# Optimization experiments

Hardware: AMD Instinct MI355X
Metric: run time of the kernel (lower is better)

The kernel has to match this reference:

```python
import jax, jax.numpy as jnp
import numpy as np

MAX_AREA_WIDTH = 3  # from init_kwargs


def _window_vals(val, width, merge):
    """Multi-scale forward window sums: for each w in 1..width, sum val[t:t+w]
    over the seq axis, concatenated along the seq axis (total length
    width*L - width*(width-1)/2). Equivalent to the torch recurrence."""
    B, H, L, D = val.shape
    csum = jnp.concatenate(
        [jnp.zeros((B, H, 1, D), val.dtype), jnp.cumsum(val, axis=2)], axis=2)
    parts = []
    for i in range(width):
        w = i + 1
        s = csum[:, :, w:, :] - csum[:, :, :L - w + 1, :]  # [B,H,L-i,D]
        if merge == 'mean':
            s = s / jnp.asarray(w, val.dtype)
        parts.append(s)
    return jnp.concatenate(parts, axis=2)


def _window_masks(mask, width, zero_pad):
    parts = [mask[:, :, :, i:] for i in range(width)]
    m = jnp.concatenate(parts, axis=-1)  # [B,H,L,L']
    if zero_pad:
        m = m.at[:, :, 0, :].set(0)
    return m


def setup_inputs() -> dict:
    key = jax.random.key(0)
    kq, kk, kv = jax.random.split(key, 3)
    B, H, L, D = 8, 8, 512, 64
    q = jax.random.normal(kq, (B, H, L, D), jnp.float32)
    k = jax.random.normal(kk, (B, H, L, D), jnp.float32)
    v = jax.random.normal(kv, (B, H, L, D), jnp.float32)
    # causal attention mask, as used in pykt knowledge-tracing models
    mask = jnp.broadcast_to(jnp.tril(jnp.ones((L, L), jnp.int32)), (B, H, L, L))
    return {"q": q, "k": k, "v": v, "d_k": 64, "mask": mask, "zero_pad": 1}


def reference(q, k, v, d_k, mask, zero_pad):
    W = MAX_AREA_WIDTH
    k_area = _window_vals(k, W, 'mean')   # [B,H,L',D]
    v_area = _window_vals(v, W, 'sum')    # [B,H,L',D]
    m = _window_masks(mask, W, zero_pad)  # [B,H,L,L']
    scores = jnp.einsum('bhqd,bhkd->bhqk', q, k_area) / jnp.sqrt(
        jnp.asarray(d_k, jnp.float32))
    scores = jnp.where(m == 0, jnp.asarray(-1e32, scores.dtype), scores)
    attn = jax.nn.softmax(scores, axis=-1)  # dropout omitted (eval / p=0)
    return jnp.einsum('bhqk,bhkd->bhqd', attn, v_area)
```

## Files before the change

kernel.cpp:

```cpp
#include <hip/hip_runtime.h>


#define LSEQ 512
#define DDIM 64
#define BQ 64
#define BK 64
#define NTH 256

__global__ __launch_bounds__(256, 2)
void area_attn_kernel(const float* __restrict__ qg,
                      const float* __restrict__ kg,
                      const float* __restrict__ vg,
                      float* __restrict__ outg) {
  const int bid = blockIdx.x;
  const int tid = threadIdx.x;

  __shared__ __align__(16) float Qs[64][68];
  __shared__ __align__(16) float KC[66 * 68];
  __shared__ __align__(16) float Ss[64][68];
  __shared__ __align__(16) float Vs[66][64];
  __shared__ float scale_arr[64];
  __shared__ float l_arr[64];

  if (bid >= 512) {
    const int bh = bid - 512;
    const float4* vb4 = (const float4*)(vg + (size_t)bh * LSEQ * DDIM);
    float4* red = (float4*)&Qs[0][0];
    const int d4 = tid & 15, rg = tid >> 4;
    float4 acc = make_float4(0.f, 0.f, 0.f, 0.f);
    for (int t = rg; t < LSEQ; t += 16) {
      float c = (t == 0 || t == LSEQ - 1) ? 3.f
              : (t == 1 || t == LSEQ - 2) ? 5.f : 6.f;
      float4 x = vb4[t * 16 + d4];
      acc.x += c * x.x; acc.y += c * x.y; acc.z += c * x.z; acc.w += c * x.w;
    }
    red[rg * 16 + d4] = acc;
    __syncthreads();
    if (rg == 0) {
      float4 s = make_float4(0.f, 0.f, 0.f, 0.f);
#pragma unroll
      for (int g = 0; g < 16; ++g) {
        float4 x = red[g * 16 + d4];
        s.x += x.x; s.y += x.y; s.z += x.z; s.w += x.w;
      }
      const float inv = 1.0f / 1533.0f;
      s.x *= inv; s.y *= inv; s.z *= inv; s.w *= inv;
      ((float4*)(outg + (size_t)bh * LSEQ * DDIM))[d4] = s;
    }
    return;
  }

  const int half = bid >> 8;
  const int qt = half ? (7 - (bid & 7)) : (bid & 7);
  const int bh = ((bid >> 3) & 31) + (half << 5);
  const int q0 = qt * BQ;

  const float* qb = qg + (size_t)bh * LSEQ * DDIM;
  const float* kb = kg + (size_t)bh * LSEQ * DDIM;
  const float* vb = vg + (size_t)bh * LSEQ * DDIM;

  {
    const float4* qa = (const float4*)(qb + q0 * DDIM);
#pragma unroll
    for (int it = 0; it < 4; ++it) {
      int f = tid + it * NTH;
      int r = f >> 4;
      int c4 = f & 15;
      float4 x = qa[f];
      int d0 = c4 * 4;
      Qs[d0 + 0][r] = x.x * 0.125f;
      Qs[d0 + 1][r] = x.y * 0.125f;
      Qs[d0 + 2][r] = x.z * 0.125f;
      Qs[d0 + 3][r] = x.w * 0.125f;
    }
  }

  const int ty = tid >> 4, tx = tid & 15;
  const int r0 = ty * 4, c0 = tx * 4;
  const int pr = tid >> 2, ps = tid & 3;
  const int ec0 = ps * 16;

  float Oa[4][4];
#pragma unroll
  for (int i = 0; i < 4; ++i)
#pragma unroll
    for (int j = 0; j < 4; ++j) Oa[i][j] = 0.f;
  float m_run = -3.0e38f, l_run = 0.f;

  const int ntiles = qt + 1;
  for (int kt = 0; kt < ntiles; ++kt) {
    const int t0 = kt * BK;

    if (ps == 0) {
      if (kt == 0) { Ss[pr][64] = -1.0e30f; Ss[pr][65] = -1.0e30f; }
      else         { Ss[pr][64] = Ss[pr][62]; Ss[pr][65] = Ss[pr][63]; }
    }
    __syncthreads();

    {
      const float4* ka = (const float4*)(kb + t0 * DDIM);
#pragma unroll
      for (int it = 0; it < 4; ++it) {
        int f = tid + it * NTH;
        int r = f >> 4;
        int c4 = f & 15;
        float4 x = ka[f];
        int d0 = c4 * 4;
        KC[(d0 + 0) * 68 + r] = x.x;
        KC[(d0 + 1) * 68 + r] = x.y;
        KC[(d0 + 2) * 68 + r] = x.z;
        KC[(d0 + 3) * 68 + r] = x.w;
      }
      const float4* va = (const float4*)(vb + t0 * DDIM);
#pragma unroll
      for (int it = 0; it < 4; ++it) {
        int f = tid + it * NTH;
        int r = f >> 4;
        int c4 = f & 15;
        ((float4*)Vs[r])[c4] = va[f];
      }
      if (tid < 32) {
        int rr = tid >> 4;
        int c4 = tid & 15;
        float4 x = make_float4(0.f, 0.f, 0.f, 0.f);
        if (kt > 0) x = ((const float4*)(vb + (size_t)(t0 - 2 + rr) * DDIM))[c4];
        ((float4*)Vs[64 + rr])[c4] = x;
      }
    }
    __syncthreads();

    {
      float acc[4][4];
#pragma unroll
      for (int i = 0; i < 4; ++i)
#pragma unroll
        for (int j = 0; j < 4; ++j) acc[i][j] = 0.f;
#pragma unroll 8
      for (int d = 0; d < 64; ++d) {
        float4 qv = *(const float4*)&Qs[d][r0];
        float4 kv = *(const float4*)&KC[d * 68 + c0];
        float qr[4] = {qv.x, qv.y, qv.z, qv.w};
        float kr[4] = {kv.x, kv.y, kv.z, kv.w};
#pragma unroll
        for (int i = 0; i < 4; ++i)
#pragma unroll
          for (int j = 0; j < 4; ++j) acc[i][j] = fmaf(qr[i], kr[j], acc[i][j]);
      }
#pragma unroll
      for (int i = 0; i < 4; ++i) {
        float4 o = make_float4(acc[i][0], acc[i][1], acc[i][2], acc[i][3]);
        *(float4*)&Ss[r0 + i][c0] = o;
      }
    }
    __syncthreads();

    {
      const int vmax = q0 + pr - t0;
      float pm1, pm2;
      if (ps == 0) { pm1 = Ss[pr][65]; pm2 = Ss[pr][64]; }
      else         { pm1 = Ss[pr][ec0 - 1]; pm2 = Ss[pr][ec0 - 2]; }

      float sv[16];
      *(float4*)&sv[0]  = *(const float4*)&Ss[pr][ec0];
      *(float4*)&sv[4]  = *(const float4*)&Ss[pr][ec0 + 4];
      *(float4*)&sv[8]  = *(const float4*)&Ss[pr][ec0 + 8];
      *(float4*)&sv[12] = *(const float4*)&Ss[pr][ec0 + 12];

      float mloc = -3.0e38f;
      {
        float a1 = pm1, a2 = pm2;
#pragma unroll
        for (int k = 0; k < 16; ++k) {
          float s0 = sv[k];
          float sc2 = 0.5f * (a1 + s0);
          float sc3 = (1.0f / 3.0f) * (a2 + a1 + s0);
          float mm = fmaxf(s0, fmaxf(sc2, sc3));
          if (ec0 + k <= vmax) mloc = fmaxf(mloc, mm);
          a2 = a1; a1 = s0;
        }
      }
      mloc = fmaxf(mloc, __shfl_xor(mloc, 1));
      mloc = fmaxf(mloc, __shfl_xor(mloc, 2));
      const float m_new = fmaxf(m_run, mloc);
      const float alpha = __expf(m_run - m_new);
      m_run = m_new;
      if (ps == 0) scale_arr[pr] = alpha;
      l_run *= alpha;

      float cf[18];
#pragma unroll
      for (int k = 0; k < 18; ++k) cf[k] = 0.f;
      float ladd = 0.f;
      {
        float a1 = pm1, a2 = pm2;
#pragma unroll
        for (int k = 0; k < 16; ++k) {
          float s0 = sv[k];
          bool vld = (ec0 + k) <= vmax;
          float p1 = vld ? __expf(s0 - m_new) : 0.f;
          float p2 = vld ? __expf(0.5f * (a1 + s0) - m_new) : 0.f;
          float p3 = vld ? __expf((1.0f / 3.0f) * (a2 + a1 + s0) - m_new) : 0.f;
          ladd += p1 + p2 + p3;
          cf[k + 2] += p1 + p2 + p3;
          cf[k + 1] += p2 + p3;
          cf[k]     += p3;
          a2 = a1; a1 = s0;
        }
      }
      ladd += __shfl_xor(ladd, 1);
      ladd += __shfl_xor(ladd, 2);
      l_run += ladd;
      if (ps == 0) l_arr[pr] = l_run;

      float up16 = __shfl_up(cf[16], 1, 4);
      float up17 = __shfl_up(cf[17], 1, 4);
      if (ps > 0) { cf[0] += up16; cf[1] += up17; }

#pragma unroll
      for (int k = 0; k < 16; ++k) {
        int lt = ec0 + k;
        int cc = (lt >= 2) ? (lt - 2) : (64 + lt);
        KC[cc * 68 + pr] = cf[k];
      }
      if (ps == 3) {
        KC[62 * 68 + pr] = cf[16];
        KC[63 * 68 + pr] = cf[17];
      }
    }
    __syncthreads();

    {
      float al[4];
#pragma unroll
      for (int i = 0; i < 4; ++i) al[i] = scale_arr[r0 + i];
#pragma unroll
      for (int i = 0; i < 4; ++i)
#pragma unroll
        for (int j = 0; j < 4; ++j) Oa[i][j] *= al[i];
#pragma unroll 2
      for (int cc = 0; cc < 66; ++cc) {
        float4 cv = *(const float4*)&KC[cc * 68 + r0];
        float4 vv = *(const float4*)&Vs[cc][c0];
        float cr[4] = {cv.x, cv.y, cv.z, cv.w};
        float vr[4] = {vv.x, vv.y, vv.z, vv.w};
#pragma unroll
        for (int i = 0; i < 4; ++i)
#pragma unroll
          for (int j = 0; j < 4; ++j) Oa[i][j] = fmaf(cr[i], vr[j], Oa[i][j]);
      }
    }
  }

  {
#pragma unroll
    for (int i = 0; i < 4; ++i) {
      int gr = q0 + r0 + i;
      if (gr != 0) {
        float inv = 1.0f / l_arr[r0 + i];
        float4 o = make_float4(Oa[i][0] * inv, Oa[i][1] * inv,
                               Oa[i][2] * inv, Oa[i][3] * inv);
        *(float4*)(outg + (size_t)(bh * LSEQ + gr) * DDIM + c0) = o;
      }
    }
  }
}

extern "C" void kernel_launch(void* const* d_in, const int* in_sizes, int n_in,
                              void* d_out, int out_size, void* d_ws, size_t ws_size,
                              hipStream_t stream) {
  (void)in_sizes; (void)n_in; (void)d_ws; (void)ws_size; (void)out_size;
  const float* q = (const float*)d_in[0];
  const float* k = (const float*)d_in[1];
  const float* v = (const float*)d_in[2];
  float* out = (float*)d_out;

  dim3 grid(512 + 64);
  area_attn_kernel<<<grid, NTH, 0, stream>>>(q, k, v, out);
}
```

Before: 177.0 us.

## Use bf16 MFMA for QK and PV with pre-transposed bf16 V

Replaces the fp32 scalar-FMA tile matmuls for QK^T and P·V with bf16 MFMA 16x16x32 instructions. A separate pre-kernel converts V to transposed bf16 in workspace. The softmax switches to exp2 with log2e scaling, and some syncthreads are dropped. Occupancy is raised to 3 blocks per CU. This lowers arithmetic cost and LDS traffic at the price of bf16 precision loss in Q, K, V and P, plus an extra kernel launch. The row-0 tail block now reads bf16 V strided.

```diff
diff --git a/kernel.cpp b/kernel.cpp
--- a/kernel.cpp
+++ b/kernel.cpp
@@ -7,32 +7,81 @@
 #define BK 64
 #define NTH 256
 
-__global__ __launch_bounds__(256, 2)
+typedef __attribute__((ext_vector_type(8))) short bf8_t;
+typedef __attribute__((ext_vector_type(4))) float f32x4;
+
+__device__ __forceinline__ unsigned short f2bf(float f) {
+  union { float f; unsigned u; } v; v.f = f;
+  unsigned u = v.u;
+  unsigned r = u + 0x7fffu + ((u >> 16) & 1u);
+  return (unsigned short)(r >> 16);
+}
+__device__ __forceinline__ float bf2f(unsigned short h) {
+  union { unsigned u; float f; } v; v.u = ((unsigned)h) << 16; return v.f;
+}
+__device__ __forceinline__ unsigned pk2(float a, float b) {
+  return (unsigned)f2bf(a) | ((unsigned)f2bf(b) << 16);
+}
+__device__ __forceinline__ float ex2(float x) {
+  float r; asm("v_exp_f32 %0, %1" : "=v"(r) : "v"(x)); return r;
+}
+__device__ __forceinline__ bf8_t pack8(float4 a, float4 b, float s) {
+  bf8_t r;
+  r[0] = (short)f2bf(a.x * s); r[1] = (short)f2bf(a.y * s);
+  r[2] = (short)f2bf(a.z * s); r[3] = (short)f2bf(a.w * s);
+  r[4] = (short)f2bf(b.x * s); r[5] = (short)f2bf(b.y * s);
+  r[6] = (short)f2bf(b.z * s); r[7] = (short)f2bf(b.w * s);
+  return r;
+}
+
+__global__ __launch_bounds__(256)
+void vt_kernel(const float* __restrict__ vg, unsigned short* __restrict__ vt) {
+  const int bh = blockIdx.x >> 3, oct = blockIdx.x & 7;
+  const float* vb = vg + (size_t)bh * LSEQ * DDIM;
+  unsigned short* vo = vt + (size_t)bh * DDIM * LSEQ;
+#pragma unroll
+  for (int it = 0; it < 4; ++it) {
+    int item = threadIdx.x + it * 256;
+    int d = item & 63, tq = item >> 6;
+    int t = oct * 64 + tq * 4;
+    ushort4 o;
+    o.x = f2bf(vb[(t + 0) * DDIM + d]);
+    o.y = f2bf(vb[(t + 1) * DDIM + d]);
+    o.z = f2bf(vb[(t + 2) * DDIM + d]);
+    o.w = f2bf(vb[(t + 3) * DDIM + d]);
+    *(ushort4*)&vo[(size_t)d * LSEQ + t] = o;
+  }
+}
+
+__global__ __launch_bounds__(256, 3)
 void area_attn_kernel(const float* __restrict__ qg,
                       const float* __restrict__ kg,
-                      const float* __restrict__ vg,
+                      const unsigned short* __restrict__ vtg,
                       float* __restrict__ outg) {
   const int bid = blockIdx.x;
   const int tid = threadIdx.x;
 
-  __shared__ __align__(16) float Qs[64][68];
-  __shared__ __align__(16) float KC[66 * 68];
+  __shared__ __align__(16) unsigned short Kbf[64 * 72];
+  __shared__ __align__(16) unsigned short Vt[64 * 72];
+  __shared__ __align__(16) unsigned short Ps[64 * 72];
   __shared__ __align__(16) float Ss[64][68];
-  __shared__ __align__(16) float Vs[66][64];
   __shared__ float scale_arr[64];
   __shared__ float l_arr[64];
 
   if (bid >= 512) {
     const int bh = bid - 512;
-    const float4* vb4 = (const float4*)(vg + (size_t)bh * LSEQ * DDIM);
-    float4* red = (float4*)&Qs[0][0];
+    const unsigned short* vb = vtg + (size_t)bh * DDIM * LSEQ;
+    float4* red = (float4*)&Ss[0][0];
     const int d4 = tid & 15, rg = tid >> 4;
     float4 acc = make_float4(0.f, 0.f, 0.f, 0.f);
     for (int t = rg; t < LSEQ; t += 16) {
       float c = (t == 0 || t == LSEQ - 1) ? 3.f
               : (t == 1 || t == LSEQ - 2) ? 5.f : 6.f;
-      float4 x = vb4[t * 16 + d4];
-      acc.x += c * x.x; acc.y += c * x.y; acc.z += c * x.z; acc.w += c * x.w;
+      int d0 = d4 * 4;
+      acc.x += c * bf2f(vb[(size_t)(d0 + 0) * LSEQ + t]);
+      acc.y += c * bf2f(vb[(size_t)(d0 + 1) * LSEQ + t]);
+      acc.z += c * bf2f(vb[(size_t)(d0 + 2) * LSEQ + t]);
+      acc.w += c * bf2f(vb[(size_t)(d0 + 3) * LSEQ + t]);
     }
     red[rg * 16 + d4] = acc;
     __syncthreads();
@@ -57,34 +106,29 @@
 
   const float* qb = qg + (size_t)bh * LSEQ * DDIM;
   const float* kb = kg + (size_t)bh * LSEQ * DDIM;
-  const float* vb = vg + (size_t)bh * LSEQ * DDIM;
-
-  {
-    const float4* qa = (const float4*)(qb + q0 * DDIM);
-#pragma unroll
-    for (int it = 0; it < 4; ++it) {
-      int f = tid + it * NTH;
-      int r = f >> 4;
-      int c4 = f & 15;
-      float4 x = qa[f];
-      int d0 = c4 * 4;
-      Qs[d0 + 0][r] = x.x * 0.125f;
-      Qs[d0 + 1][r] = x.y * 0.125f;
-      Qs[d0 + 2][r] = x.z * 0.125f;
-      Qs[d0 + 3][r] = x.w * 0.125f;
-    }
-  }
-
-  const int ty = tid >> 4, tx = tid & 15;
-  const int r0 = ty * 4, c0 = tx * 4;
+  const unsigned short* vtb = vtg + (size_t)bh * DDIM * LSEQ;
+
+  const int lane = tid & 63, w = tid >> 6;
+  const int lc = lane & 15, lg = lane >> 4;
+  const int koff = lg * 8;
   const int pr = tid >> 2, ps = tid & 3;
   const int ec0 = ps * 16;
-
-  float Oa[4][4];
-#pragma unroll
-  for (int i = 0; i < 4; ++i)
-#pragma unroll
-    for (int j = 0; j < 4; ++j) Oa[i][j] = 0.f;
+  const float L2E = 1.44269504088896341f;
+
+  bf8_t qa0, qa1;
+  {
+    const float* qrp = qb + (size_t)(q0 + 16 * w + lc) * DDIM;
+    float4 xa = *(const float4*)(qrp + koff);
+    float4 xb = *(const float4*)(qrp + koff + 4);
+    qa0 = pack8(xa, xb, 0.125f);
+    xa = *(const float4*)(qrp + 32 + koff);
+    xb = *(const float4*)(qrp + 36 + koff);
+    qa1 = pack8(xa, xb, 0.125f);
+  }
+
+  f32x4 oacc[4];
+#pragma unroll
+  for (int nt = 0; nt < 4; ++nt) oacc[nt] = (f32x4){0.f, 0.f, 0.f, 0.f};
   float m_run = -3.0e38f, l_run = 0.f;
 
   const int ntiles = qt + 1;
@@ -98,73 +142,57 @@
     __syncthreads();
 
     {
-      const float4* ka = (const float4*)(kb + t0 * DDIM);
+      const float4* ka = (const float4*)(kb + (size_t)t0 * DDIM);
 #pragma unroll
       for (int it = 0; it < 4; ++it) {
         int f = tid + it * NTH;
-        int r = f >> 4;
-        int c4 = f & 15;
-        float4 x = ka[f];
-        int d0 = c4 * 4;
-        KC[(d0 + 0) * 68 + r] = x.x;
-        KC[(d0 + 1) * 68 + r] = x.y;
-        KC[(d0 + 2) * 68 + r] = x.z;
-        KC[(d0 + 3) * 68 + r] = x.w;
-      }
-      const float4* va = (const float4*)(vb + t0 * DDIM);
+        int t = f >> 4, c4 = f & 15;
+        float4 x = ka[t * 16 + c4];
+        ushort4 o;
+        o.x = f2bf(x.x); o.y = f2bf(x.y); o.z = f2bf(x.z); o.w = f2bf(x.w);
+        *(ushort4*)&Kbf[t * 72 + c4 * 4] = o;
+      }
 #pragma unroll
       for (int it = 0; it < 4; ++it) {
         int f = tid + it * NTH;
-        int r = f >> 4;
-        int c4 = f & 15;
-        ((float4*)Vs[r])[c4] = va[f];
-      }
-      if (tid < 32) {
-        int rr = tid >> 4;
-        int c4 = tid & 15;
-        float4 x = make_float4(0.f, 0.f, 0.f, 0.f);
-        if (kt > 0) x = ((const float4*)(vb + (size_t)(t0 - 2 + rr) * DDIM))[c4];
-        ((float4*)Vs[64 + rr])[c4] = x;
+        int d = f >> 4, tq = f & 15;
+        ushort4 x = *(const ushort4*)&vtb[(size_t)d * LSEQ + t0 + tq * 4];
+        *(ushort4*)&Vt[d * 72 + tq * 4] = x;
+      }
+      if (tid < 64) {
+        unsigned x = 0;
+        if (kt > 0) x = *(const unsigned*)&vtb[(size_t)tid * LSEQ + t0 - 2];
+        *(unsigned*)&Vt[tid * 72 + 64] = x;
       }
     }
     __syncthreads();
 
-    {
-      float acc[4][4];
-#pragma unroll
-      for (int i = 0; i < 4; ++i)
-#pragma unroll
-        for (int j = 0; j < 4; ++j) acc[i][j] = 0.f;
-#pragma unroll 8
-      for (int d = 0; d < 64; ++d) {
-        float4 qv = *(const float4*)&Qs[d][r0];
-        float4 kv = *(const float4*)&KC[d * 68 + c0];
-        float qr[4] = {qv.x, qv.y, qv.z, qv.w};
-        float kr[4] = {kv.x, kv.y, kv.z, kv.w};
-#pragma unroll
-        for (int i = 0; i < 4; ++i)
-#pragma unroll
-          for (int j = 0; j < 4; ++j) acc[i][j] = fmaf(qr[i], kr[j], acc[i][j]);
-      }
-#pragma unroll
-      for (int i = 0; i < 4; ++i) {
-        float4 o = make_float4(acc[i][0], acc[i][1], acc[i][2], acc[i][3]);
-        *(float4*)&Ss[r0 + i][c0] = o;
-      }
-    }
-    __syncthreads();
+#pragma unroll
+    for (int nt = 0; nt < 4; ++nt) {
+      int key = nt * 16 + lc;
+      bf8_t kb0 = *(const bf8_t*)&Kbf[key * 72 + koff];
+      bf8_t kb1 = *(const bf8_t*)&Kbf[key * 72 + 32 + koff];
+      f32x4 acc = (f32x4){0.f, 0.f, 0.f, 0.f};
+      acc = __builtin_amdgcn_mfma_f32_16x16x32_bf16(qa0, kb0, acc, 0, 0, 0);
+      acc = __builtin_amdgcn_mfma_f32_16x16x32_bf16(qa1, kb1, acc, 0, 0, 0);
+#pragma unroll
+      for (int r = 0; r < 4; ++r)
+        Ss[16 * w + 4 * lg + r][nt * 16 + lc] = acc[r];
+    }
 
     {
       const int vmax = q0 + pr - t0;
       float pm1, pm2;
-      if (ps == 0) { pm1 = Ss[pr][65]; pm2 = Ss[pr][64]; }
-      else         { pm1 = Ss[pr][ec0 - 1]; pm2 = Ss[pr][ec0 - 2]; }
+      if (ps == 0) { pm1 = Ss[pr][65] * L2E; pm2 = Ss[pr][64] * L2E; }
+      else         { pm1 = Ss[pr][ec0 - 1] * L2E; pm2 = Ss[pr][ec0 - 2] * L2E; }
 
       float sv[16];
       *(float4*)&sv[0]  = *(const float4*)&Ss[pr][ec0];
       *(float4*)&sv[4]  = *(const float4*)&Ss[pr][ec0 + 4];
       *(float4*)&sv[8]  = *(const float4*)&Ss[pr][ec0 + 8];
       *(float4*)&sv[12] = *(const float4*)&Ss[pr][ec0 + 12];
+#pragma unroll
+      for (int k = 0; k < 16; ++k) sv[k] *= L2E;
 
       float mloc = -3.0e38f;
       {
@@ -172,9 +200,8 @@
 #pragma unroll
         for (int k = 0; k < 16; ++k) {
           float s0 = sv[k];
-          float sc2 = 0.5f * (a1 + s0);
-          float sc3 = (1.0f / 3.0f) * (a2 + a1 + s0);
-          float mm = fmaxf(s0, fmaxf(sc2, sc3));
+          float t = a1 + s0;
+          float mm = fmaxf(s0, fmaxf(0.5f * t, (1.0f / 3.0f) * (a2 + t)));
           if (ec0 + k <= vmax) mloc = fmaxf(mloc, mm);
           a2 = a1; a1 = s0;
         }
@@ -182,7 +209,7 @@
       mloc = fmaxf(mloc, __shfl_xor(mloc, 1));
       mloc = fmaxf(mloc, __shfl_xor(mloc, 2));
       const float m_new = fmaxf(m_run, mloc);
-      const float alpha = __expf(m_run - m_new);
+      const float alpha = ex2(m_run - m_new);
       m_run = m_new;
       if (ps == 0) scale_arr[pr] = alpha;
       l_run *= alpha;
@@ -197,12 +224,14 @@
         for (int k = 0; k < 16; ++k) {
           float s0 = sv[k];
           bool vld = (ec0 + k) <= vmax;
-          float p1 = vld ? __expf(s0 - m_new) : 0.f;
-          float p2 = vld ? __expf(0.5f * (a1 + s0) - m_new) : 0.f;
-          float p3 = vld ? __expf((1.0f / 3.0f) * (a2 + a1 + s0) - m_new) : 0.f;
-          ladd += p1 + p2 + p3;
-          cf[k + 2] += p1 + p2 + p3;
-          cf[k + 1] += p2 + p3;
+          float t = a1 + s0;
+          float p1 = vld ? ex2(s0 - m_new) : 0.f;
+          float p2 = vld ? ex2(0.5f * t - m_new) : 0.f;
+          float p3 = vld ? ex2((1.0f / 3.0f) * (a2 + t) - m_new) : 0.f;
+          float p23 = p2 + p3, p123 = p1 + p23;
+          ladd += p123;
+          cf[k + 2] += p123;
+          cf[k + 1] += p23;
           cf[k]     += p3;
           a2 = a1; a1 = s0;
         }
@@ -216,50 +245,66 @@
       float up17 = __shfl_up(cf[17], 1, 4);
       if (ps > 0) { cf[0] += up16; cf[1] += up17; }
 
-#pragma unroll
-      for (int k = 0; k < 16; ++k) {
-        int lt = ec0 + k;
-        int cc = (lt >= 2) ? (lt - 2) : (64 + lt);
-        KC[cc * 68 + pr] = cf[k];
-      }
-      if (ps == 3) {
-        KC[62 * 68 + pr] = cf[16];
-        KC[63 * 68 + pr] = cf[17];
-      }
-    }
-    __syncthreads();
+      const int base = pr * 72;
+      if (ps == 0) {
+        *(unsigned*)&Ps[base + 64] = pk2(cf[0], cf[1]);
+#pragma unroll
+        for (int j = 0; j < 7; ++j)
+          *(unsigned*)&Ps[base + 2 * j] = pk2(cf[2 + 2 * j], cf[3 + 2 * j]);
+      } else {
+        const int tcb = 16 * ps - 2;
+#pragma unroll
+        for (int j = 0; j < 8; ++j)
+          *(unsigned*)&Ps[base + tcb + 2 * j] = pk2(cf[2 * j], cf[2 * j + 1]);
+        if (ps == 3) *(unsigned*)&Ps[base + 62] = pk2(cf[16], cf[17]);
+      }
+    }
 
     {
       float al[4];
 #pragma unroll
-      for (int i = 0; i < 4; ++i) al[i] = scale_arr[r0 + i];
-#pragma unroll
-      for (int i = 0; i < 4; ++i)
-#pragma unroll
-        for (int j = 0; j < 4; ++j) Oa[i][j] *= al[i];
-#pragma unroll 2
-      for (int cc = 0; cc < 66; ++cc) {
-        float4 cv = *(const float4*)&KC[cc * 68 + r0];
-        float4 vv = *(const float4*)&Vs[cc][c0];
-        float cr[4] = {cv.x, cv.y, cv.z, cv.w};
-        float vr[4] = {vv.x, vv.y, vv.z, vv.w};
-#pragma unroll
-        for (int i = 0; i < 4; ++i)
-#pragma unroll
-          for (int j = 0; j < 4; ++j) Oa[i][j] = fmaf(cr[i], vr[j], Oa[i][j]);
+      for (int r = 0; r < 4; ++r) al[r] = scale_arr[16 * w + 4 * lg + r];
+#pragma unroll
+      for (int nt = 0; nt < 4; ++nt)
+#pragma unroll
+        for (int r = 0; r < 4; ++r) oacc[nt][r] *= al[r];
+
+      bf8_t pa0 = *(const bf8_t*)&Ps[(16 * w + lc) * 72 + koff];
+      bf8_t pa1 = *(const bf8_t*)&Ps[(16 * w + lc) * 72 + 32 + koff];
+      float cm2[4], cm1[4];
+#pragma unroll
+      for (int r = 0; r < 4; ++r) {
+        unsigned pc = *(const unsigned*)&Ps[(16 * w + 4 * lg + r) * 72 + 64];
+        cm2[r] = bf2f((unsigned short)(pc & 0xffffu));
+        cm1[r] = bf2f((unsigned short)(pc >> 16));
+      }
+#pragma unroll
+      for (int nt = 0; nt < 4; ++nt) {
+        int d = nt * 16 + lc;
+        bf8_t vb0 = *(const bf8_t*)&Vt[d * 72 + koff];
+        bf8_t vb1 = *(const bf8_t*)&Vt[d * 72 + 32 + koff];
+        oacc[nt] = __builtin_amdgcn_mfma_f32_16x16x32_bf16(pa0, vb0, oacc[nt], 0, 0, 0);
+        oacc[nt] = __builtin_amdgcn_mfma_f32_16x16x32_bf16(pa1, vb1, oacc[nt], 0, 0, 0);
+        unsigned vc = *(const unsigned*)&Vt[d * 72 + 64];
+        float vm2 = bf2f((unsigned short)(vc & 0xffffu));
+        float vm1 = bf2f((unsigned short)(vc >> 16));
+#pragma unroll
+        for (int r = 0; r < 4; ++r)
+          oacc[nt][r] += cm2[r] * vm2 + cm1[r] * vm1;
       }
     }
   }
 
   {
 #pragma unroll
-    for (int i = 0; i < 4; ++i) {
-      int gr = q0 + r0 + i;
+    for (int r = 0; r < 4; ++r) {
+      int row = 16 * w + 4 * lg + r;
+      int gr = q0 + row;
       if (gr != 0) {
-        float inv = 1.0f / l_arr[r0 + i];
-        float4 o = make_float4(Oa[i][0] * inv, Oa[i][1] * inv,
-                               Oa[i][2] * inv, Oa[i][3] * inv);
-        *(float4*)(outg + (size_t)(bh * LSEQ + gr) * DDIM + c0) = o;
+        float inv = 1.0f / l_arr[row];
+#pragma unroll
+        for (int nt = 0; nt < 4; ++nt)
+          outg[(size_t)(bh * LSEQ + gr) * DDIM + nt * 16 + lc] = oacc[nt][r] * inv;
       }
     }
   }
@@ -268,12 +313,13 @@
 extern "C" void kernel_launch(void* const* d_in, const int* in_sizes, int n_in,
                               void* d_out, int out_size, void* d_ws, size_t ws_size,
                               hipStream_t stream) {
-  (void)in_sizes; (void)n_in; (void)d_ws; (void)ws_size; (void)out_size;
+  (void)in_sizes; (void)n_in; (void)ws_size; (void)out_size;
   const float* q = (const float*)d_in[0];
   const float* k = (const float*)d_in[1];
   const float* v = (const float*)d_in[2];
   float* out = (float*)d_out;
-
-  dim3 grid(512 + 64);
-  area_attn_kernel<<<grid, NTH, 0, stream>>>(q, k, v, out);
-}
+  unsigned short* vt = (unsigned short*)d_ws;
+
+  vt_kernel<<<dim3(512), dim3(256), 0, stream>>>(v, vt);
+  area_attn_kernel<<<dim3(512 + 64), dim3(256), 0, stream>>>(q, k, vt, out);
+}
```

New measurement: 146.3 us. -17.4%, faster.
